# Performance work log

Measured on AMD Instinct MI355X. Metric: run time of the kernel, lower is better.

Reference implementation:

```python
import jax, jax.numpy as jnp
import numpy as np
import itertools

EPSILON = 1e-7
SIGMA_BOOST = 2.0
IN_NUM = 50000
OUT_NUM = 50000
K = 131072
ADDITIONAL = 12
SIGMA_SCALE = 0.2
FEAT = 128
RANK = 2

# floor mask: itertools.product([True, False], repeat=2) -> (4, 2)
FLOOR_MASK = jnp.asarray(
    [[bool(b) for b in bools] for bools in itertools.product([True, False], repeat=RANK)]
)


def setup_inputs() -> dict:
    key = jax.random.key(0)
    k1, k2, k3a, k3b = jax.random.split(key, 4)
    params = jax.random.normal(k1, (K, 4), dtype=jnp.float32)
    x = jax.random.normal(k2, (IN_NUM, FEAT), dtype=jnp.float32)
    # sampled ints: floor(uniform * (1-eps) * rng_dim), per dim
    s0 = jax.random.randint(k3a, (K, ADDITIONAL, 1), 0, OUT_NUM)
    s1 = jax.random.randint(k3b, (K, ADDITIONAL, 1), 0, IN_NUM)
    sampled_ints = jnp.concatenate([s0, s1], axis=-1).astype(jnp.int32)
    return {"params": params, "x": x, "sampled_ints": sampled_ints}


def _hyper(params):
    size = jnp.asarray([OUT_NUM, IN_NUM], dtype=params.dtype)  # (2,)
    means = jax.nn.sigmoid(params[:, 0:RANK]) * (size - 1.0)   # (K, 2)
    sigmas = (jax.nn.softplus(params[:, RANK:RANK + 1] + SIGMA_BOOST) + EPSILON)  # (K, 1)
    sigmas = sigmas * size * SIGMA_SCALE                        # (K, 2)
    values = jax.nn.sigmoid(params[:, RANK + 1])                # (K,)
    return means, sigmas, values


def reference(params, x, sampled_ints):
    means, sigmas, values = _hyper(params)

    # neighbor integer index tuples: floor/ceil combinations -> (K, 4, 2)
    m = means[:, None, :]  # (K, 1, 2)
    neighbor_ints = jnp.where(FLOOR_MASK[None], jnp.floor(m), jnp.ceil(m)).astype(jnp.int32)
    ints = jnp.concatenate([neighbor_ints, sampled_ints], axis=1)  # (K, D, 2)
    ints_fl = ints.astype(means.dtype)

    # unnormalized Gaussian densities of each int tuple under its MVN
    inv_std = jnp.sqrt(1.0 / (EPSILON + sigmas))[:, None, :]      # (K, 1, 2)
    diff = (ints_fl - means[:, None, :]) * inv_std                # (K, D, 2)
    props = jnp.exp(-0.5 * jnp.sum(diff * diff, axis=-1))         # (K, D)
    props = props / jnp.sum(props + EPSILON, axis=1, keepdims=True)

    vals = (values[:, None] * props).reshape(-1)                  # (K*D,)
    i_ixs = ints[:, :, 0].reshape(-1)                             # row indices
    j_ixs = ints[:, :, 1].reshape(-1)                             # col indices

    # sparse (OUT_NUM, IN_NUM) @ x  ->  (OUT_NUM, FEAT)
    gathered = x[j_ixs] * vals[:, None]                           # (nnz, FEAT)
    out = jax.ops.segment_sum(gathered, i_ixs, num_segments=OUT_NUM)
    return out
```

## Files before the change

kernel.cpp:

```cpp
#include <hip/hip_runtime.h>
#include <math.h>

constexpr int KT       = 131072;
constexpr int IN_NUM_C = 50000;
constexpr int OUT_NUM_C= 50000;
constexpr int FEAT_C   = 128;
constexpr int ADD_C    = 12;
constexpr int NP       = 16;
constexpr float EPS    = 1e-7f;
constexpr int CAP      = 128;

__device__ __forceinline__ float xla_expf(float x) {
    const float LOG2EF = 1.44269504088896341f;
    const float C1 =  0.693359375f;
    const float C2 = -2.12194440e-4f;
    const float P0 = 1.9875691500e-4f;
    const float P1 = 1.3981999507e-3f;
    const float P2 = 8.3334519073e-3f;
    const float P3 = 4.1665795894e-2f;
    const float P4 = 1.6666665459e-1f;
    const float P5 = 5.0000001201e-1f;

    const float fx = floorf(__fadd_rn(__fmul_rn(x, LOG2EF), 0.5f));
    const float tmp = __fmul_rn(C1, fx);
    const float z2  = __fmul_rn(C2, fx);
    float r = __fsub_rn(x, tmp);
    r       = __fsub_rn(r, z2);
    const float r2 = __fmul_rn(r, r);

    float y = __fadd_rn(__fmul_rn(r, P0), P1);
    y = __fadd_rn(__fmul_rn(y, r), P2);
    y = __fadd_rn(__fmul_rn(y, r), P3);
    y = __fadd_rn(__fmul_rn(y, r), P4);
    y = __fadd_rn(__fmul_rn(y, r), P5);
    y = __fadd_rn(__fmul_rn(y, r2), r);
    y = __fadd_rn(1.0f, y);

    const int e = (int)fx;
    const float s = __int_as_float((e + 127) << 23);
    const float res = __fmul_rn(y, s);
    return fmaxf(res, x);
}

__device__ __forceinline__ float sigmoid_xla_f32(float p) {
    const float t = xla_expf(-p);
    const float d = __fadd_rn(1.0f, t);
    return __fdiv_rn(1.0f, d);
}


__global__ __launch_bounds__(256) void append_kernel(
    const float* __restrict__ params,
    const int*   __restrict__ samp,
    int*         __restrict__ counts,
    uint2*       __restrict__ sorted)
{
    const int k = blockIdx.x * 16 + (threadIdx.x >> 4);
    const int s = threadIdx.x & 15;

    const float4 p = ((const float4*)params)[k];

    const float m0 = __fmul_rn(sigmoid_xla_f32(p.x), (float)(OUT_NUM_C - 1));
    const float m1 = __fmul_rn(sigmoid_xla_f32(p.y), (float)(IN_NUM_C  - 1));
    const int fl0 = (int)floorf(m0), ce0 = (int)ceilf(m0);
    const int fl1 = (int)floorf(m1), ce1 = (int)ceilf(m1);

    const float z  = p.z + 2.0f;
    const float sp = fmaxf(z, 0.0f) + log1pf(expf(-fabsf(z))) + 1e-7f;
    const float is0 = rsqrtf(1e-7f + sp * (OUT_NUM_C * 0.2f));
    const float is1 = rsqrtf(1e-7f + sp * (IN_NUM_C  * 0.2f));
    const float value = 1.0f / (1.0f + expf(-p.w));

    int iv, jv;
    if (s < 4) {
        iv = (s < 2)        ? fl0 : ce0;
        jv = ((s & 1) == 0) ? fl1 : ce1;
    } else {
        const int base = (k * ADD_C + (s - 4)) * 2;
        iv = samp[base + 0];
        jv = samp[base + 1];
    }
    const float d0 = ((float)iv - m0) * is0;
    const float d1 = ((float)jv - m1) * is1;
    const float prop = expf(-0.5f * (d0 * d0 + d1 * d1));

    float ssum = prop;
    #pragma unroll
    for (int off = 1; off < 16; off <<= 1)
        ssum += __shfl_xor(ssum, off, 64);
    const float denom = ssum + (float)NP * EPS;
    const float w = value * prop / denom;

    if (w != 0.0f) {
        const int pos = atomicAdd(&counts[iv], 1);
        if (pos < CAP)
            sorted[(size_t)iv * CAP + pos] = make_uint2((unsigned)jv, __float_as_uint(w));
    }
}

__global__ __launch_bounds__(256) void gather_cap_kernel(
    const uint2* __restrict__ sorted,
    const int*   __restrict__ counts,
    const float* __restrict__ x,
    float*       __restrict__ out)
{
    const int wv   = threadIdx.x >> 6;
    const int lane = threadIdx.x & 63;
    const int row  = blockIdx.x * 4 + wv;
    const int quad = lane >> 4;
    const int fi   = (lane & 15) << 3;
    const int n    = counts[row];
    const uint2* rowp = sorted + (size_t)row * CAP;

    float4 a0 = make_float4(0.f, 0.f, 0.f, 0.f);
    float4 a1 = make_float4(0.f, 0.f, 0.f, 0.f);

    for (int base = 0; base < n; base += 64) {
        uint2 ent = make_uint2(0u, 0u);
        if (base + lane < n) ent = rowp[base + lane];
        const int m  = min(64, n - base);
        const int mq = (m + 3) >> 2;
        int t = quad;
        #pragma unroll 2
        for (int it = 0; it < mq; ++it, t += 4) {
            const int   j = __shfl((int)ent.x, t, 64);
            const float w = __uint_as_float(__shfl((int)ent.y, t, 64));
            const float* xp = x + (size_t)j * FEAT_C + fi;
            const float4 v0 = *(const float4*)(xp);
            const float4 v1 = *(const float4*)(xp + 4);
            a0.x = fmaf(w, v0.x, a0.x);  a0.y = fmaf(w, v0.y, a0.y);
            a0.z = fmaf(w, v0.z, a0.z);  a0.w = fmaf(w, v0.w, a0.w);
            a1.x = fmaf(w, v1.x, a1.x);  a1.y = fmaf(w, v1.y, a1.y);
            a1.z = fmaf(w, v1.z, a1.z);  a1.w = fmaf(w, v1.w, a1.w);
        }
    }
    #pragma unroll
    for (int off = 16; off < 64; off <<= 1) {
        a0.x += __shfl_xor(a0.x, off, 64);  a0.y += __shfl_xor(a0.y, off, 64);
        a0.z += __shfl_xor(a0.z, off, 64);  a0.w += __shfl_xor(a0.w, off, 64);
        a1.x += __shfl_xor(a1.x, off, 64);  a1.y += __shfl_xor(a1.y, off, 64);
        a1.z += __shfl_xor(a1.z, off, 64);  a1.w += __shfl_xor(a1.w, off, 64);
    }
    if (quad == 0) {
        float* op = out + (size_t)row * FEAT_C + fi;
        *(float4*)(op)     = a0;
        *(float4*)(op + 4) = a1;
    }
}

__global__ __launch_bounds__(256) void hist_kernel(
    const float* __restrict__ params,
    const int*   __restrict__ samp,
    int*         __restrict__ hist)
{
    const int e = blockIdx.x * 256 + threadIdx.x;
    const int k = e >> 4, s = e & 15;
    int iv;
    if (s < 4) {
        const float m0 = __fmul_rn(sigmoid_xla_f32(params[k * 4 + 0]),
                                   (float)(OUT_NUM_C - 1));
        iv = (s < 2) ? (int)floorf(m0) : (int)ceilf(m0);
    } else {
        iv = samp[(k * ADD_C + (s - 4)) * 2];
    }
    atomicAdd(&hist[iv], 1);
}

__global__ __launch_bounds__(1024) void scan_kernel(
    const int* __restrict__ hist,
    int*       __restrict__ offs,
    int*       __restrict__ cursor)
{
    __shared__ int lsum[1024];
    const int t = threadIdx.x;
    const int CH = 49;
    const int lo = t * CH;
    const int hi = min(lo + CH, OUT_NUM_C);
    int s = 0;
    for (int i = lo; i < hi; ++i) s += hist[i];
    lsum[t] = s;
    __syncthreads();
    for (int off = 1; off < 1024; off <<= 1) {
        const int v = (t >= off) ? lsum[t - off] : 0;
        __syncthreads();
        lsum[t] += v;
        __syncthreads();
    }
    int run = (t > 0) ? lsum[t - 1] : 0;
    for (int i = lo; i < hi; ++i) {
        offs[i] = run; cursor[i] = run;
        run += hist[i];
    }
    if (t == 1023) offs[OUT_NUM_C] = lsum[1023];
}

__global__ __launch_bounds__(256) void scatter_kernel(
    const float* __restrict__ params,
    const int*   __restrict__ samp,
    int*         __restrict__ cursor,
    uint2*       __restrict__ sorted)
{
    const int wave = threadIdx.x >> 6;
    const int lane = threadIdx.x & 63;
    const int k    = blockIdx.x * 4 + wave;

    const float p0 = params[k * 4 + 0];
    const float p1 = params[k * 4 + 1];
    const float p2 = params[k * 4 + 2];
    const float p3 = params[k * 4 + 3];

    const float m0 = __fmul_rn(sigmoid_xla_f32(p0), (float)(OUT_NUM_C - 1));
    const float m1 = __fmul_rn(sigmoid_xla_f32(p1), (float)(IN_NUM_C  - 1));
    const int fl0 = (int)floorf(m0), ce0 = (int)ceilf(m0);
    const int fl1 = (int)floorf(m1), ce1 = (int)ceilf(m1);

    const double z  = (double)p2 + 2.0;
    const double sp = fmax(z, 0.0) + log1p(exp(-fabs(z))) + 1e-7;
    const float is0 = (float)sqrt(1.0 / (1e-7 + sp * (OUT_NUM_C * 0.2)));
    const float is1 = (float)sqrt(1.0 / (1e-7 + sp * (IN_NUM_C  * 0.2)));
    const float value = (float)(1.0 / (1.0 + exp(-(double)p3)));

    const int s = lane & 15;
    int iv, jv;
    if (s < 4) {
        iv = (s < 2)        ? fl0 : ce0;
        jv = ((s & 1) == 0) ? fl1 : ce1;
    } else {
        const int base = (k * ADD_C + (s - 4)) * 2;
        iv = samp[base + 0];
        jv = samp[base + 1];
    }
    const float d0 = ((float)iv - m0) * is0;
    const float d1 = ((float)jv - m1) * is1;
    const float prop = expf(-0.5f * (d0 * d0 + d1 * d1));

    float ssum = prop;
    #pragma unroll
    for (int off = 1; off < 64; off <<= 1)
        ssum += __shfl_xor(ssum, off, 64);
    const float denom = ssum * 0.25f + (float)NP * EPS;
    const float w = value * prop / denom;

    if (lane < 16) {
        const int pos = atomicAdd(&cursor[iv], 1);
        sorted[pos] = make_uint2((unsigned)jv, __float_as_uint(w));
    }
}

__global__ __launch_bounds__(64) void gather_kernel(
    const uint2* __restrict__ sorted,
    const int*   __restrict__ offs,
    const float* __restrict__ x,
    float*       __restrict__ out)
{
    const int row  = blockIdx.x;
    const int lane = threadIdx.x;
    const int half = lane >> 5;
    const int fl   = (lane & 31) << 2;
    const int beg = offs[row], end = offs[row + 1];
    float4 acc = make_float4(0.f, 0.f, 0.f, 0.f);
    for (int base = beg; base < end; base += 64) {
        uint2 ent = make_uint2(0u, 0u);
        if (base + lane < end) ent = sorted[base + lane];
        const int n  = min(64, end - base);
        const int nh = (n + 1) >> 1;
        int t = half;
        #pragma unroll 2
        for (int it = 0; it < nh; ++it, t += 2) {
            const int   j = __shfl((int)ent.x, t, 64);
            const float w = __uint_as_float(__shfl((int)ent.y, t, 64));
            const float4 xv = *(const float4*)(x + (size_t)j * FEAT_C + fl);
            acc.x = fmaf(w, xv.x, acc.x);
            acc.y = fmaf(w, xv.y, acc.y);
            acc.z = fmaf(w, xv.z, acc.z);
            acc.w = fmaf(w, xv.w, acc.w);
        }
    }
    acc.x += __shfl_xor(acc.x, 32, 64);
    acc.y += __shfl_xor(acc.y, 32, 64);
    acc.z += __shfl_xor(acc.z, 32, 64);
    acc.w += __shfl_xor(acc.w, 32, 64);
    if (half == 0)
        *(float4*)(out + (size_t)row * FEAT_C + fl) = acc;
}

__global__ __launch_bounds__(256) void mh_scatter_kernel(
    const float* __restrict__ params,
    const float* __restrict__ x,
    const int*   __restrict__ samp,
    float*       __restrict__ out)
{
    const int wave = threadIdx.x >> 6;
    const int lane = threadIdx.x & 63;
    const int k    = blockIdx.x * 4 + wave;

    const float p0 = params[k * 4 + 0];
    const float p1 = params[k * 4 + 1];
    const float p2 = params[k * 4 + 2];
    const float p3 = params[k * 4 + 3];

    const float m0 = __fmul_rn(sigmoid_xla_f32(p0), (float)(OUT_NUM_C - 1));
    const float m1 = __fmul_rn(sigmoid_xla_f32(p1), (float)(IN_NUM_C  - 1));
    const int fl0 = (int)floorf(m0), ce0 = (int)ceilf(m0);
    const int fl1 = (int)floorf(m1), ce1 = (int)ceilf(m1);

    const double z  = (double)p2 + 2.0;
    const double sp = fmax(z, 0.0) + log1p(exp(-fabs(z))) + 1e-7;
    const float is0 = (float)sqrt(1.0 / (1e-7 + sp * (OUT_NUM_C * 0.2)));
    const float is1 = (float)sqrt(1.0 / (1e-7 + sp * (IN_NUM_C  * 0.2)));
    const float value = (float)(1.0 / (1.0 + exp(-(double)p3)));

    const int s = lane & 15;
    int iv, jv;
    if (s < 4) {
        iv = (s < 2)        ? fl0 : ce0;
        jv = ((s & 1) == 0) ? fl1 : ce1;
    } else {
        const int base = (k * ADD_C + (s - 4)) * 2;
        iv = samp[base + 0];
        jv = samp[base + 1];
    }
    const float d0 = ((float)iv - m0) * is0;
    const float d1 = ((float)jv - m1) * is1;
    const float prop = expf(-0.5f * (d0 * d0 + d1 * d1));

    float ssum = prop;
    #pragma unroll
    for (int off = 1; off < 64; off <<= 1)
        ssum += __shfl_xor(ssum, off, 64);
    const float denom = ssum * 0.25f + (float)NP * EPS;
    const float w = value * prop / denom;

    const int f = lane * 2;
    #pragma unroll 1
    for (int t = 0; t < NP; ++t) {
        const float wt = __shfl(w,  t, 64);
        const int   it = __shfl(iv, t, 64);
        const int   jt = __shfl(jv, t, 64);
        const float2 xv = *(const float2*)(x + (size_t)jt * FEAT_C + f);
        float* op = out + (size_t)it * FEAT_C + f;
        atomicAdd(op + 0, xv.x * wt);
        atomicAdd(op + 1, xv.y * wt);
    }
}

extern "C" void kernel_launch(void* const* d_in, const int* in_sizes, int n_in,
                              void* d_out, int out_size, void* d_ws, size_t ws_size,
                              hipStream_t stream)
{
    const float* params = (const float*)d_in[0];
    const float* x      = (const float*)d_in[1];
    const int*   samp   = (const int*)  d_in[2];
    float*       out    = (float*)d_out;

    const size_t CNT_OFF  = 0;
    const size_t BKT_OFF  = 256 * 1024;
    const size_t NEED_CAP = BKT_OFF + (size_t)OUT_NUM_C * CAP * sizeof(uint2);

    const size_t HIST_OFF = 0;
    const size_t OFFS_OFF = 256 * 1024;
    const size_t CURS_OFF = 512 * 1024;
    const size_t SORT_OFF = 768 * 1024;
    const size_t NEED_CS  = SORT_OFF + (size_t)KT * NP * sizeof(uint2);

    if (ws_size >= NEED_CAP) {
        int*   counts = (int*)  ((char*)d_ws + CNT_OFF);
        uint2* sorted = (uint2*)((char*)d_ws + BKT_OFF);
        hipMemsetAsync(counts, 0, OUT_NUM_C * sizeof(int), stream);
        append_kernel    <<<KT / 16,       256, 0, stream>>>(params, samp, counts, sorted);
        gather_cap_kernel<<<OUT_NUM_C / 4, 256, 0, stream>>>(sorted, counts, x, out);
    } else if (ws_size >= NEED_CS) {
        int*   hist   = (int*)  ((char*)d_ws + HIST_OFF);
        int*   offs   = (int*)  ((char*)d_ws + OFFS_OFF);
        int*   cursor = (int*)  ((char*)d_ws + CURS_OFF);
        uint2* sorted = (uint2*)((char*)d_ws + SORT_OFF);
        hipMemsetAsync(hist, 0, (OUT_NUM_C + 1) * sizeof(int), stream);
        hist_kernel   <<<KT * NP / 256, 256,  0, stream>>>(params, samp, hist);
        scan_kernel   <<<1,             1024, 0, stream>>>(hist, offs, cursor);
        scatter_kernel<<<KT / 4,        256,  0, stream>>>(params, samp, cursor, sorted);
        gather_kernel <<<OUT_NUM_C,     64,   0, stream>>>(sorted, offs, x, out);
    } else {
        hipMemsetAsync(out, 0, (size_t)out_size * sizeof(float), stream);
        mh_scatter_kernel<<<KT / 4, 256, 0, stream>>>(params, x, samp, out);
    }
}
```

Baseline: 127.1 us.

## Process all sixteen entries of a parameter row in a single thread

The append kernel now maps one thread to each parameter row instead of sixteen threads per row. Each thread computes the row's hyperparameters once, loads its sampled index pairs with vectorized int4 reads, sums the densities in registers instead of by shuffle reduction, and issues sixteen atomic appends itself. This removes the sixteen-fold repeated sigmoid and softplus work and the cross-lane reduction. In exchange the grid has sixteen times fewer threads, so occupancy and latency hiding are much lower, and each thread's atomics and stores now run in sequence.

```diff
diff --git a/kernel.cpp b/kernel.cpp
--- a/kernel.cpp
+++ b/kernel.cpp
@@ -55,8 +55,7 @@
     int*         __restrict__ counts,
     uint2*       __restrict__ sorted)
 {
-    const int k = blockIdx.x * 16 + (threadIdx.x >> 4);
-    const int s = threadIdx.x & 15;
+    const int k = blockIdx.x * 256 + threadIdx.x;
 
     const float4 p = ((const float4*)params)[k];
 
@@ -71,30 +70,45 @@
     const float is1 = rsqrtf(1e-7f + sp * (IN_NUM_C  * 0.2f));
     const float value = 1.0f / (1.0f + expf(-p.w));
 
-    int iv, jv;
-    if (s < 4) {
-        iv = (s < 2)        ? fl0 : ce0;
-        jv = ((s & 1) == 0) ? fl1 : ce1;
-    } else {
-        const int base = (k * ADD_C + (s - 4)) * 2;
-        iv = samp[base + 0];
-        jv = samp[base + 1];
-    }
-    const float d0 = ((float)iv - m0) * is0;
-    const float d1 = ((float)jv - m1) * is1;
-    const float prop = expf(-0.5f * (d0 * d0 + d1 * d1));
-
-    float ssum = prop;
-    #pragma unroll
-    for (int off = 1; off < 16; off <<= 1)
-        ssum += __shfl_xor(ssum, off, 64);
+    const int4* sp4 = (const int4*)(samp + (size_t)k * ADD_C * 2);
+    int4 sv[6];
+    #pragma unroll
+    for (int i = 0; i < 6; ++i) sv[i] = sp4[i];
+
+    int   ivs[NP], jvs[NP];
+    float props[NP];
+    #pragma unroll
+    for (int e = 0; e < 4; ++e) {
+        ivs[e] = (e < 2)        ? fl0 : ce0;
+        jvs[e] = ((e & 1) == 0) ? fl1 : ce1;
+    }
+    #pragma unroll
+    for (int i = 0; i < 6; ++i) {
+        ivs[4 + 2*i]     = sv[i].x;  jvs[4 + 2*i]     = sv[i].y;
+        ivs[4 + 2*i + 1] = sv[i].z;  jvs[4 + 2*i + 1] = sv[i].w;
+    }
+
+    float ssum = 0.0f;
+    #pragma unroll
+    for (int e = 0; e < NP; ++e) {
+        const float d0 = ((float)ivs[e] - m0) * is0;
+        const float d1 = ((float)jvs[e] - m1) * is1;
+        props[e] = expf(-0.5f * (d0 * d0 + d1 * d1));
+        ssum += props[e];
+    }
     const float denom = ssum + (float)NP * EPS;
-    const float w = value * prop / denom;
-
-    if (w != 0.0f) {
-        const int pos = atomicAdd(&counts[iv], 1);
-        if (pos < CAP)
-            sorted[(size_t)iv * CAP + pos] = make_uint2((unsigned)jv, __float_as_uint(w));
+    const float vd = value / denom;
+
+    #pragma unroll
+    for (int e = 0; e < NP; ++e) {
+        const float w = vd * props[e];
+        if (w != 0.0f) {
+            const int iv = ivs[e];
+            const int pos = atomicAdd(&counts[iv], 1);
+            if (pos < CAP)
+                sorted[(size_t)iv * CAP + pos] =
+                    make_uint2((unsigned)jvs[e], __float_as_uint(w));
+        }
     }
 }
 
@@ -367,7 +381,7 @@
         int*   counts = (int*)  ((char*)d_ws + CNT_OFF);
         uint2* sorted = (uint2*)((char*)d_ws + BKT_OFF);
         hipMemsetAsync(counts, 0, OUT_NUM_C * sizeof(int), stream);
-        append_kernel    <<<KT / 16,       256, 0, stream>>>(params, samp, counts, sorted);
+        append_kernel    <<<KT / 256,      256, 0, stream>>>(params, samp, counts, sorted);
         gather_cap_kernel<<<OUT_NUM_C / 4, 256, 0, stream>>>(sorted, counts, x, out);
     } else if (ws_size >= NEED_CS) {
         int*   hist   = (int*)  ((char*)d_ws + HIST_OFF);
```

After: 137.7 us. +8.4%, slower.
